# Kernel optimization log

Measured on AMD Instinct MI355X. Metric: run time of the kernel, lower is better.

Reference implementation:

```python
import jax, jax.numpy as jnp
import numpy as np

B, S, D, H = 4, 2048, 512, 8
KD = D // H          # key_dim == head_dim == 64
FFN = 4 * D

def _ln(x, g, b, eps):
    mu = x.mean(-1, keepdims=True)
    var = ((x - mu) ** 2).mean(-1, keepdims=True)
    return (x - mu) / jnp.sqrt(var + eps) * g + b

def setup_inputs():
    key = jax.random.key(0)
    ks = jax.random.split(key, 8)
    def lin(k, o, i, scale=0.02):
        k1, k2 = jax.random.split(k)
        return (jax.random.normal(k1, (o, i), jnp.float32) * scale,
                jax.random.normal(k2, (o,), jnp.float32) * scale)
    wq, bq = lin(ks[0], D, D)
    wk, bk = lin(ks[1], D, D)
    wv, bv = lin(ks[2], D, D)
    wg, bg = lin(ks[3], D, D)
    wo, bo = lin(ks[4], D, D)
    fc1_w, fc1_b = lin(ks[5], FFN, D)
    fc2_w, fc2_b = lin(ks[6], D, FFN)
    return {
        'src': jax.random.normal(ks[7], (B, S, D), jnp.float32),
        'mask': jnp.zeros((S, S), jnp.bool_),
        'padding_mask': jnp.zeros((B, S), jnp.bool_),
        'wq': wq, 'bq': bq, 'wk': wk, 'bk': bk, 'wv': wv, 'bv': bv,
        'wg': wg, 'bg': bg, 'wo': wo, 'bo': bo,
        'fc1_w': fc1_w, 'fc1_b': fc1_b, 'fc2_w': fc2_w, 'fc2_b': fc2_b,
        'ln_ffn_g': jnp.ones((FFN,), jnp.float32), 'ln_ffn_b': jnp.zeros((FFN,), jnp.float32),
        'n0_g': jnp.ones((D,), jnp.float32), 'n0_b': jnp.zeros((D,), jnp.float32),
        'n1_g': jnp.ones((D,), jnp.float32), 'n1_b': jnp.zeros((D,), jnp.float32),
    }

def reference(src, mask, padding_mask, wq, bq, wk, bk, wv, bv, wg, bg, wo, bo,
              fc1_w, fc1_b, fc2_w, fc2_b, ln_ffn_g, ln_ffn_b, n0_g, n0_b, n1_g, n1_b):
    b, s, d = src.shape
    # RetNet per-head decay mask (h, s, s): exp((i-j)*log(gamma_h)) on the lower triangle,
    # row-normalized by sqrt(row sum) (torchscale RetNetRelPos, parallel mode).
    idx = jnp.arange(s)
    diff = (idx[:, None] - idx[None, :]).astype(src.dtype)
    decay = jnp.log(1.0 - 2.0 ** (-5.0 - jnp.arange(H, dtype=src.dtype)))
    dm = jnp.where(diff[None] >= 0, jnp.exp(diff[None] * decay[:, None, None]), 0.0)
    dm = dm / jnp.sqrt(dm.sum(-1, keepdims=True))
    # projections; k scaled by key_dim**-0.5 before head split
    q = (src @ wq.T + bq).reshape(b, s, H, KD).transpose(0, 2, 1, 3)
    k = ((src @ wk.T + bk) * (KD ** -0.5)).reshape(b, s, H, KD).transpose(0, 2, 1, 3)
    v = src @ wv.T + bv
    g = src @ wg.T + bg
    # parallel retention: additive decay bias, detached L1 row normalization
    qk = jnp.einsum('bhid,bhjd->bhij', q, k) + dm[None]
    den = jnp.maximum(jnp.abs(jax.lax.stop_gradient(qk).sum(-1, keepdims=True)), 1.0)
    qk = qk / den
    vr = v.reshape(b, s, H, KD).transpose(0, 2, 1, 3)
    o = jnp.einsum('bhij,bhjd->bhid', qk, vr).transpose(0, 2, 1, 3)  # (b,s,h,hd)
    # per-head LayerNorm, eps=1e-6, no affine
    mu = o.mean(-1, keepdims=True)
    o = (o - mu) / jnp.sqrt(((o - mu) ** 2).mean(-1, keepdims=True) + 1e-6)
    o = jax.nn.silu(g) * o.reshape(b, s, d)
    o = o @ wo.T + bo
    # post-norm residual layout
    x = _ln(src + o, n0_g, n0_b, 1e-5)
    h = jax.nn.gelu(x @ fc1_w.T + fc1_b, approximate=False)
    h = _ln(h, ln_ffn_g, ln_ffn_b, 1e-6)  # subln
    h = h @ fc2_w.T + fc2_b
    return _ln(x + h, n1_g, n1_b, 1e-5)
```

## Files before the change

kernel.cpp:

```cpp
#include <hip/hip_runtime.h>
#include <hip/hip_bf16.h>
#include <math.h>

#define DEV __device__ __forceinline__

typedef __attribute__((ext_vector_type(4))) float f32x4;
typedef __attribute__((ext_vector_type(16))) float f32x16;
typedef __attribute__((ext_vector_type(8))) short bf16x8;
typedef __attribute__((ext_vector_type(8))) unsigned short u16x8;
typedef unsigned short u16;
typedef unsigned int u32;

DEV u16 f2bf(float f) {
  union { float f; u32 u; } v; v.f = f;
  u32 r = v.u + 0x7fffu + ((v.u >> 16) & 1u);
  return (u16)(r >> 16);
}
DEV float bf2f(u16 h) {
  union { u32 u; float f; } v; v.u = ((u32)h) << 16;
  return v.f;
}
DEV float bfel(bf16x8 v, int e) {
  union { bf16x8 b; u16x8 u; } x; x.b = v; return bf2f(x.u[e]);
}

DEV void gl_lds16(const u16* g, u16* s) {
  __builtin_amdgcn_global_load_lds((const __attribute__((address_space(1))) void*)g,
                                   (__attribute__((address_space(3))) void*)s, 16, 0, 0);
}

DEV void barrier_() {
  __builtin_amdgcn_sched_barrier(0);
  asm volatile("" ::: "memory");
  __builtin_amdgcn_s_barrier();
  asm volatile("" ::: "memory");
  __builtin_amdgcn_sched_barrier(0);
}

#define MFMA16(a, b, c) __builtin_amdgcn_mfma_f32_16x16x32_bf16((a), (b), (c), 0, 0, 0)
#define MFMA32(a, b, c) __builtin_amdgcn_mfma_f32_32x32x16_bf16((a), (b), (c), 0, 0, 0)

DEV void cast8(const float* in, u16* out, float s) {
  f32x4 a = *(const f32x4*)in;
  f32x4 b = *(const f32x4*)(in + 4);
  u16x8 r;
  r[0] = f2bf(a[0] * s); r[1] = f2bf(a[1] * s); r[2] = f2bf(a[2] * s); r[3] = f2bf(a[3] * s);
  r[4] = f2bf(b[0] * s); r[5] = f2bf(b[1] * s); r[6] = f2bf(b[2] * s); r[7] = f2bf(b[3] * s);
  *(u16x8*)out = r;
}

__global__ __launch_bounds__(256) void prep_cast(
    const float* __restrict__ src, const float* __restrict__ wq, const float* __restrict__ wk,
    const float* __restrict__ wv, const float* __restrict__ wg, const float* __restrict__ wo,
    const float* __restrict__ fc1, const float* __restrict__ fc2,
    const float* __restrict__ bq, const float* __restrict__ bk,
    const float* __restrict__ bv, const float* __restrict__ bg,
    u16* __restrict__ src_bf, u16* __restrict__ Wcat, u16* __restrict__ wo_bf,
    u16* __restrict__ fc1_bf, u16* __restrict__ fc2_bf, float* __restrict__ bcat) {
  int u = blockIdx.x * 256 + threadIdx.x;
  if (u < 524288) {
    cast8(src + (size_t)u * 8, src_bf + (size_t)u * 8, 1.0f);
  } else if (u < 557056) {
    int v = u - 524288; cast8(wq + (size_t)v * 8, Wcat + (size_t)v * 8, 1.0f);
  } else if (u < 589824) {
    int v = u - 557056; cast8(wk + (size_t)v * 8, Wcat + 262144 + (size_t)v * 8, 0.125f);
  } else if (u < 622592) {
    int v = u - 589824; cast8(wv + (size_t)v * 8, Wcat + 524288 + (size_t)v * 8, 1.0f);
  } else if (u < 655360) {
    int v = u - 622592; cast8(wg + (size_t)v * 8, Wcat + 786432 + (size_t)v * 8, 1.0f);
  } else if (u < 688128) {
    int v = u - 655360; cast8(wo + (size_t)v * 8, wo_bf + (size_t)v * 8, 1.0f);
  } else if (u < 819200) {
    int v = u - 688128; cast8(fc1 + (size_t)v * 8, fc1_bf + (size_t)v * 8, 1.0f);
  } else if (u < 950272) {
    int v = u - 819200; cast8(fc2 + (size_t)v * 8, fc2_bf + (size_t)v * 8, 1.0f);
  } else if (u < 950528) {
    int v = u - 950272;
    #pragma unroll
    for (int e = 0; e < 8; e++) {
      int c = v * 8 + e;
      float val;
      if (c < 512)       val = bq[c];
      else if (c < 1024) val = bk[c - 512] * 0.125f;
      else if (c < 1536) val = bv[c - 1024];
      else               val = bg[c - 1536];
      bcat[c] = val;
    }
  }
}

template <int ACT>
__global__ __launch_bounds__(256) void gemm_v4(
    const u16* __restrict__ A, const u16* __restrict__ W, const float* __restrict__ bias,
    u16* __restrict__ Ob, int N, int K, int TN) {
  __shared__ __align__(16) u16 sm[16384];
  const int t = threadIdx.x, l = t & 63;
  const int w = t >> 6, wr = (w >> 1) * 64, wc = (w & 1) * 64;
  const int lc = l & 15, lch = l >> 4;
  const int NT = K >> 5;

  const int orig = blockIdx.x;
  const int cpx = gridDim.x >> 3;
  const int sid = (orig & 7) * cpx + (orig >> 3);
  const int bm = (sid / TN) * 128, bn = (sid % TN) * 128;

  const int srow = t >> 2, sc = t & 3;
  const int soff = (sc ^ ((srow >> 1) & 3)) * 8;
  const u16* stA = A + (size_t)(bm + srow) * K + soff;
  const u16* stB = W + (size_t)(bn + srow) * K + soff;
  const size_t rstep = (size_t)64 * K;

#define STAGE(bidx, kt)                                   \
  {                                                       \
    u16* d = sm + (bidx) * 8192 + t * 8;                  \
    gl_lds16(stA + (kt), d);                              \
    gl_lds16(stA + rstep + (kt), d + 2048);               \
    gl_lds16(stB + (kt), d + 4096);                       \
    gl_lds16(stB + rstep + (kt), d + 6144);               \
  }

  f32x4 acc[4][4] = {};
  STAGE(0, 0)

  const int key = (lch ^ ((lc >> 1) & 3)) * 8;
  for (int tt = 0; tt < NT; ++tt) {
    if (tt + 1 < NT) {
      STAGE((tt + 1) & 1, (tt + 1) * 32)
      asm volatile("s_waitcnt vmcnt(4)" ::: "memory");
    } else {
      asm volatile("s_waitcnt vmcnt(0)" ::: "memory");
    }
    barrier_();
    const u16* bufp = sm + (tt & 1) * 8192;
    bf16x8 af[4], bfv[4];
    #pragma unroll
    for (int mi = 0; mi < 4; mi++)
      af[mi] = *(const bf16x8*)&bufp[(wr + mi * 16 + lc) * 32 + key];
    #pragma unroll
    for (int ni = 0; ni < 4; ni++)
      bfv[ni] = *(const bf16x8*)&bufp[4096 + (wc + ni * 16 + lc) * 32 + key];
    #pragma unroll
    for (int mi = 0; mi < 4; mi++)
      #pragma unroll
      for (int ni = 0; ni < 4; ni++)
        acc[mi][ni] = MFMA16(af[mi], bfv[ni], acc[mi][ni]);
    asm volatile("s_waitcnt lgkmcnt(0)" ::: "memory");
    barrier_();
  }
#undef STAGE

  u16* osm = sm;
  #pragma unroll
  for (int ni = 0; ni < 4; ni++) {
    const int col = wc + ni * 16 + lc;
    const float bb = bias[bn + col];
    const int ckey = col >> 3, clow = col & 7;
    #pragma unroll
    for (int mi = 0; mi < 4; mi++) {
      #pragma unroll
      for (int r = 0; r < 4; r++) {
        const int row = wr + mi * 16 + lch * 4 + r;
        float v = acc[mi][ni][r] + bb;
        if (ACT == 1) v = 0.5f * v * (1.0f + erff(v * 0.70710678118f));
        osm[row * 128 + ((ckey ^ ((row & 7) << 1)) << 3) + clow] = f2bf(v);
      }
    }
  }
  __syncthreads();
  #pragma unroll
  for (int p = 0; p < 8; p++) {
    const int flat = p * 256 + t;
    const int row = flat >> 4, c = flat & 15;
    u16x8 y = *(const u16x8*)&osm[row * 128 + ((c ^ ((row & 7) << 1)) << 3)];
    *(u16x8*)&Ob[(size_t)(bm + row) * N + bn + c * 8] = y;
  }
}

template <int ACT>
__global__ __launch_bounds__(256) void gemm_m64_v4(
    const u16* __restrict__ A, const u16* __restrict__ W, const float* __restrict__ bias,
    u16* __restrict__ Ob, int N, int K, int TN) {
  __shared__ __align__(16) u16 sm[12288];
  const int t = threadIdx.x, l = t & 63;
  const int w = t >> 6, wr = (w >> 1) * 32, wc = (w & 1) * 64;
  const int lc = l & 15, lch = l >> 4;
  const int NT = K >> 5;

  const int orig = blockIdx.x;
  const int cpx = gridDim.x >> 3;
  const int sid = (orig & 7) * cpx + (orig >> 3);
  const int bm = (sid / TN) * 64, bn = (sid % TN) * 128;

  const int srow = t >> 2, sc = t & 3;
  const int soff = (sc ^ ((srow >> 1) & 3)) * 8;
  const u16* stA = A + (size_t)(bm + srow) * K + soff;
  const u16* stB = W + (size_t)(bn + srow) * K + soff;
  const size_t rstep = (size_t)64 * K;

#define STAGE(bidx, kt)                                   \
  {                                                       \
    u16* d = sm + (bidx) * 6144 + t * 8;                  \
    gl_lds16(stA + (kt), d);                              \
    gl_lds16(stB + (kt), d + 2048);                       \
    gl_lds16(stB + rstep + (kt), d + 4096);               \
  }

  f32x4 acc[2][4] = {};
  STAGE(0, 0)

  const int key = (lch ^ ((lc >> 1) & 3)) * 8;
  for (int tt = 0; tt < NT; ++tt) {
    if (tt + 1 < NT) {
      STAGE((tt + 1) & 1, (tt + 1) * 32)
      asm volatile("s_waitcnt vmcnt(3)" ::: "memory");
    } else {
      asm volatile("s_waitcnt vmcnt(0)" ::: "memory");
    }
    barrier_();
    const u16* bufp = sm + (tt & 1) * 6144;
    bf16x8 af[2], bfv[4];
    #pragma unroll
    for (int mi = 0; mi < 2; mi++)
      af[mi] = *(const bf16x8*)&bufp[(wr + mi * 16 + lc) * 32 + key];
    #pragma unroll
    for (int ni = 0; ni < 4; ni++)
      bfv[ni] = *(const bf16x8*)&bufp[2048 + (wc + ni * 16 + lc) * 32 + key];
    #pragma unroll
    for (int mi = 0; mi < 2; mi++)
      #pragma unroll
      for (int ni = 0; ni < 4; ni++)
        acc[mi][ni] = MFMA16(af[mi], bfv[ni], acc[mi][ni]);
    asm volatile("s_waitcnt lgkmcnt(0)" ::: "memory");
    barrier_();
  }
#undef STAGE

  u16* osm = sm;
  #pragma unroll
  for (int ni = 0; ni < 4; ni++) {
    const int col = wc + ni * 16 + lc;
    const float bb = bias[bn + col];
    const int ckey = col >> 3, clow = col & 7;
    #pragma unroll
    for (int mi = 0; mi < 2; mi++) {
      #pragma unroll
      for (int r = 0; r < 4; r++) {
        const int row = wr + mi * 16 + lch * 4 + r;
        float v = acc[mi][ni][r] + bb;
        if (ACT == 1) v = 0.5f * v * (1.0f + erff(v * 0.70710678118f));
        osm[row * 128 + ((ckey ^ ((row & 7) << 1)) << 3) + clow] = f2bf(v);
      }
    }
  }
  __syncthreads();
  #pragma unroll
  for (int p = 0; p < 4; p++) {
    const int flat = p * 256 + t;
    const int row = flat >> 4, c = flat & 15;
    u16x8 y = *(const u16x8*)&osm[row * 128 + ((c ^ ((row & 7) << 1)) << 3)];
    *(u16x8*)&Ob[(size_t)(bm + row) * N + bn + c * 8] = y;
  }
}

__global__ __launch_bounds__(256) void transkv(
    const u16* __restrict__ qkvg, u16* __restrict__ ktg, u16* __restrict__ vtg,
    float* __restrict__ Wtab) {
  __shared__ u16 Lk[64 * 72], Lv[64 * 72];
  const int t = threadIdx.x;
  const int bh = blockIdx.x, c = blockIdx.y, b = bh >> 3, h = bh & 7;
  const int jt = c * 64;
  const u16* kptr = qkvg + (size_t)(b * 2048 + jt) * 2048 + 512 + h * 64;
  const u16* vptr = kptr + 512;
  const int r0 = t >> 3, c0 = (t & 7) * 8;
  u16x8 k0 = *(const u16x8*)(kptr + (size_t)r0 * 2048 + c0);
  u16x8 k1 = *(const u16x8*)(kptr + (size_t)(r0 + 32) * 2048 + c0);
  u16x8 v0 = *(const u16x8*)(vptr + (size_t)r0 * 2048 + c0);
  u16x8 v1 = *(const u16x8*)(vptr + (size_t)(r0 + 32) * 2048 + c0);
  #pragma unroll
  for (int e = 0; e < 8; e++) {
    Lk[(c0 + e) * 72 + r0] = k0[e];  Lk[(c0 + e) * 72 + 32 + r0] = k1[e];
    Lv[(c0 + e) * 72 + r0] = v0[e];  Lv[(c0 + e) * 72 + 32 + r0] = v1[e];
  }
  __syncthreads();
  {
    u16* kd = ktg + (size_t)bh * 64 * 2048 + jt;
    u16* vd = vtg + (size_t)bh * 64 * 2048 + jt;
    *(u16x8*)(kd + (size_t)r0 * 2048 + c0)        = *(const u16x8*)&Lk[r0 * 72 + c0];
    *(u16x8*)(kd + (size_t)(r0 + 32) * 2048 + c0) = *(const u16x8*)&Lk[(r0 + 32) * 72 + c0];
    *(u16x8*)(vd + (size_t)r0 * 2048 + c0)        = *(const u16x8*)&Lv[r0 * 72 + c0];
    *(u16x8*)(vd + (size_t)(r0 + 32) * 2048 + c0) = *(const u16x8*)&Lv[(r0 + 32) * 72 + c0];
  }
  if (t < 64) {
    const float gamma = 1.0f - exp2f(-5.0f - (float)h);
    float acc = 0.0f, p = 1.0f;
    for (int jj = 0; jj < 64; jj++) {
      acc += p * bf2f(Lv[t * 72 + (63 - jj)]);
      p *= gamma;
    }
    Wtab[((size_t)bh * 32 + c) * 64 + t] = acc;
  }
}

__global__ __launch_bounds__(256) void scan_kernel(
    const u16* __restrict__ ktg, float* __restrict__ Ctab, float* __restrict__ ksum) {
  __shared__ float ps[4][64];
  const int t = threadIdx.x, bh = blockIdx.x, h = bh & 7;
  const int a = t & 63, q = t >> 6;
  const u16* kr = ktg + (size_t)bh * 64 * 2048 + (size_t)a * 2048 + q * 512;
  float s = 0.0f;
  for (int j = 0; j < 512; j += 8) {
    u16x8 v = *(const u16x8*)(kr + j);
    #pragma unroll
    for (int e = 0; e < 8; e++) s += bf2f(v[e]);
  }
  ps[q][a] = s;
  __syncthreads();
  if (t < 64) {
    ksum[bh * 64 + t] = ps[0][t] + ps[1][t] + ps[2][t] + ps[3][t];
    const float gamma = 1.0f - exp2f(-5.0f - (float)h);
    const float g64 = exp2f(64.0f * log2f(gamma));
    float* Wp = Ctab + (size_t)bh * 32 * 64 + t;
    float C = 0.0f;
    for (int c = 0; c < 32; c++) {
      C = C * g64 + Wp[c * 64];
      Wp[c * 64] = C;
    }
  }
}

__global__ __launch_bounds__(256) void vtk_kernel(
    const u16* __restrict__ vtg, const u16* __restrict__ ktg, u16* __restrict__ vtk) {
  __shared__ float red[3][4096];
  const int t = threadIdx.x, l = t & 63, w = t >> 6;
  const int bh = blockIdx.x;
  const int lc = l & 15, lch = l >> 4;
  const u16* vb = vtg + (size_t)bh * 64 * 2048;
  const u16* kb = ktg + (size_t)bh * 64 * 2048;
  f32x4 acc[4][4] = {};
  for (int it = 0; it < 16; ++it) {
    const int j0 = w * 512 + it * 32 + lch * 8;
    bf16x8 af[4], bfr[4];
    #pragma unroll
    for (int mt = 0; mt < 4; mt++)
      af[mt] = *(const bf16x8*)(vb + (size_t)(mt * 16 + lc) * 2048 + j0);
    #pragma unroll
    for (int nt = 0; nt < 4; nt++)
      bfr[nt] = *(const bf16x8*)(kb + (size_t)(nt * 16 + lc) * 2048 + j0);
    #pragma unroll
    for (int mt = 0; mt < 4; mt++)
      #pragma unroll
      for (int nt = 0; nt < 4; nt++)
        acc[mt][nt] = MFMA16(af[mt], bfr[nt], acc[mt][nt]);
  }
  if (w > 0) {
    #pragma unroll
    for (int mt = 0; mt < 4; mt++)
      #pragma unroll
      for (int nt = 0; nt < 4; nt++)
        #pragma unroll
        for (int r = 0; r < 4; r++)
          red[w - 1][(mt * 16 + lch * 4 + r) * 64 + nt * 16 + lc] = acc[mt][nt][r];
  }
  __syncthreads();
  if (w == 0) {
    u16* out = vtk + (size_t)bh * 64 * 64;
    #pragma unroll
    for (int mt = 0; mt < 4; mt++)
      #pragma unroll
      for (int nt = 0; nt < 4; nt++)
        #pragma unroll
        for (int r = 0; r < 4; r++) {
          int row = mt * 16 + lch * 4 + r, col = nt * 16 + lc;
          float v = acc[mt][nt][r] + red[0][row * 64 + col] + red[1][row * 64 + col] +
                    red[2][row * 64 + col];
          out[row * 64 + col] = f2bf(v);
        }
  }
}

__global__ __launch_bounds__(512) void ret_out(
    const u16* __restrict__ qkvg, const u16* __restrict__ vtg,
    const u16* __restrict__ vtk, const float* __restrict__ Ctab,
    const float* __restrict__ ksum, u16* __restrict__ gated) {
  const int S = 2048, DD = 2048;
  const int bh = blockIdx.x, b = bh >> 3, h = bh & 7;
  const int t = threadIdx.x, l = t & 63, w = t >> 6;
  const int lid = l & 31, hi = l >> 5;
  const int wrow = blockIdx.y * 256 + w * 32;
  const int i_q = wrow + lid;
  const int chunk = wrow >> 6;
  const int iloc = i_q & 63;

  __shared__ __align__(16) u16 sm[18432];
  float* smf = (float*)sm;

  const size_t base = (size_t)b * S * DD + (size_t)h * 64;
  const u16* qp = qkvg + base;
  const u16* gp = qkvg + base + 1536;

  const float gamma = 1.0f - exp2f(-5.0f - (float)h);
  const float l2g = log2f(gamma);
  const float rowsum = (1.0f - exp2f((float)(i_q + 1) * l2g)) * exp2f(5.0f + (float)h);
  const float rrs = rsqrtf(rowsum);

  {
    const int il = t >> 3, j0 = (t & 7) * 8;
    u16x8 row;
    #pragma unroll
    for (int e = 0; e < 8; e++) {
      int d = il - (j0 + e);
      row[e] = (d >= 0) ? f2bf(exp2f((float)d * l2g)) : (u16)0;
    }
    *(u16x8*)&sm[il * 72 + j0] = row;
  }
  if (t < 256) {
    int cc = blockIdx.y * 4 - 1 + (t >> 6);
    smf[4608 + t] = (cc >= 0) ? Ctab[((size_t)bh * 32 + cc) * 64 + (t & 63)] : 0.0f;
  } else if (t < 320) {
    smf[4864 + (t - 256)] = ksum[bh * 64 + (t - 256)];
  }
  __syncthreads();

  bf16x8 qf[4];
  #pragma unroll
  for (int kc = 0; kc < 4; kc++)
    qf[kc] = *(const bf16x8*)(qp + (size_t)i_q * DD + kc * 16 + 8 * hi);

  const u16* vt_b = vtg + (size_t)bh * 64 * S;
  const u16* vk_b = vtk + (size_t)bh * 64 * 64;

  f32x16 accO0, accO1;
  #pragma unroll
  for (int r = 0; r < 16; r++) { accO0[r] = 0.0f; accO1[r] = 0.0f; }

  #pragma unroll
  for (int kc = 0; kc < 4; kc++) {
    bf16x8 lb = *(const bf16x8*)&sm[iloc * 72 + kc * 16 + hi * 8];
    bf16x8 va0 = *(const bf16x8*)(vt_b + (size_t)lid * S + chunk * 64 + kc * 16 + hi * 8);
    bf16x8 va1 = *(const bf16x8*)(vt_b + (size_t)(lid + 32) * S + chunk * 64 + kc * 16 + hi * 8);
    accO0 = MFMA32(va0, lb, accO0);
    accO1 = MFMA32(va1, lb, accO1);
  }
  {
    const float gpw = exp2f((float)(iloc + 1) * l2g);
    const float* Cst = &smf[4608 + (w >> 1) * 64];
    #pragma unroll
    for (int r = 0; r < 16; r++) {
      int br = (r & 3) + 8 * (r >> 2) + 4 * hi;
      accO0[r] += gpw * Cst[br];
      accO1[r] += gpw * Cst[32 + br];
    }
  }
  #pragma unroll
  for (int r = 0; r < 16; r++) { accO0[r] *= rrs; accO1[r] *= rrs; }
  #pragma unroll
  for (int kc = 0; kc < 4; kc++) {
    bf16x8 ka0 = *(const bf16x8*)(vk_b + (size_t)lid * 64 + kc * 16 + hi * 8);
    bf16x8 ka1 = *(const bf16x8*)(vk_b + (size_t)(lid + 32) * 64 + kc * 16 + hi * 8);
    accO0 = MFMA32(ka0, qf[kc], accO0);
    accO1 = MFMA32(ka1, qf[kc], accO1);
  }
  float dsum = 0.0f;
  #pragma unroll
  for (int kc = 0; kc < 4; kc++) {
    const float* Ks = &smf[4864 + kc * 16 + hi * 8];
    #pragma unroll
    for (int e = 0; e < 8; e++) dsum += bfel(qf[kc], e) * Ks[e];
  }
  dsum += __shfl_xor(dsum, 32);
  float den = dsum + sqrtf(rowsum);
  float rden = 1.0f / fmaxf(fabsf(den), 1.0f);

  float o0[16], o1[16];
  float s1 = 0.0f, s2 = 0.0f;
  #pragma unroll
  for (int r = 0; r < 16; r++) {
    o0[r] = accO0[r] * rden; s1 += o0[r]; s2 += o0[r] * o0[r];
    o1[r] = accO1[r] * rden; s1 += o1[r]; s2 += o1[r] * o1[r];
  }
  s1 += __shfl_xor(s1, 32);
  s2 += __shfl_xor(s2, 32);
  float mu = s1 * (1.0f / 64.0f);
  float var = s2 * (1.0f / 64.0f) - mu * mu;
  float rv = rsqrtf(var + 1e-6f);

  __syncthreads();

  u16* Ot = sm + w * 2304;
  #pragma unroll
  for (int r = 0; r < 16; r++) {
    int d = (r & 3) + 8 * (r >> 2) + 4 * hi;
    Ot[lid * 72 + d]      = f2bf((o0[r] - mu) * rv);
    Ot[lid * 72 + 32 + d] = f2bf((o1[r] - mu) * rv);
  }
  {
    const int i2 = l >> 1, half = l & 1;
    const int row = wrow + i2;
    #pragma unroll
    for (int c = 0; c < 4; c++) {
      u16x8 y8 = *(const u16x8*)&Ot[i2 * 72 + half * 32 + c * 8];
      u16x8 g8 = *(const u16x8*)(gp + (size_t)row * DD + half * 32 + c * 8);
      u16x8 o8;
      #pragma unroll
      for (int e = 0; e < 8; e++) {
        float gv = bf2f(g8[e]);
        float sg = gv / (1.0f + __expf(-gv));
        o8[e] = f2bf(bf2f(y8[e]) * sg);
      }
      *(u16x8*)&gated[((size_t)(b * S + row)) * 512 + h * 64 + half * 32 + c * 8] = o8;
    }
  }
}

template <int AF32, int WF>
__global__ __launch_bounds__(256) void add_lnT(
    const void* __restrict__ Ap, const u16* __restrict__ Bv,
    const float* __restrict__ gam, const float* __restrict__ bet, float eps,
    float* __restrict__ Of, u16* __restrict__ Ob) {
  int row = blockIdx.x * 4 + (threadIdx.x >> 6);
  int l = threadIdx.x & 63;
  float x[8];
  u16x8 cv = *(const u16x8*)(Bv + (size_t)row * 512 + l * 8);
  if (AF32) {
    const float* a = (const float*)Ap + (size_t)row * 512 + l * 8;
    f32x4 a0 = *(const f32x4*)a, a1 = *(const f32x4*)(a + 4);
    #pragma unroll
    for (int e = 0; e < 4; e++) { x[e] = a0[e] + bf2f(cv[e]); x[4 + e] = a1[e] + bf2f(cv[4 + e]); }
  } else {
    u16x8 av = *(const u16x8*)((const u16*)Ap + (size_t)row * 512 + l * 8);
    #pragma unroll
    for (int e = 0; e < 8; e++) x[e] = bf2f(av[e]) + bf2f(cv[e]);
  }
  float s = 0.f, s2 = 0.f;
  #pragma unroll
  for (int e = 0; e < 8; e++) { s += x[e]; s2 += x[e] * x[e]; }
  #pragma unroll
  for (int m = 1; m <= 32; m <<= 1) { s += __shfl_xor(s, m); s2 += __shfl_xor(s2, m); }
  float mu = s * (1.0f / 512.0f);
  float var = s2 * (1.0f / 512.0f) - mu * mu;
  float rinv = rsqrtf(var + eps);
  f32x4 g0 = *(const f32x4*)(gam + l * 8), g1 = *(const f32x4*)(gam + l * 8 + 4);
  f32x4 b0 = *(const f32x4*)(bet + l * 8), b1 = *(const f32x4*)(bet + l * 8 + 4);
  f32x4 y0, y1;
  #pragma unroll
  for (int e = 0; e < 4; e++) {
    y0[e] = (x[e] - mu) * rinv * g0[e] + b0[e];
    y1[e] = (x[4 + e] - mu) * rinv * g1[e] + b1[e];
  }
  if (WF) {
    float* op = Of + (size_t)row * 512 + l * 8;
    *(f32x4*)op = y0;
    *(f32x4*)(op + 4) = y1;
  }
  if (Ob) {
    u16x8 rb_;
    #pragma unroll
    for (int e = 0; e < 4; e++) { rb_[e] = f2bf(y0[e]); rb_[4 + e] = f2bf(y1[e]); }
    *(u16x8*)(Ob + (size_t)row * 512 + l * 8) = rb_;
  }
}

__global__ __launch_bounds__(256) void subln_ffn(
    u16* __restrict__ hbuf, const float* __restrict__ gam, const float* __restrict__ bet) {
  int row = blockIdx.x * 4 + (threadIdx.x >> 6);
  int l = threadIdx.x & 63;
  u16* p = hbuf + (size_t)row * 2048;
  float x[32];
  #pragma unroll
  for (int cch = 0; cch < 4; cch++) {
    u16x8 v = *(const u16x8*)(p + cch * 512 + l * 8);
    #pragma unroll
    for (int e = 0; e < 8; e++) x[cch * 8 + e] = bf2f(v[e]);
  }
  float s = 0.f, s2 = 0.f;
  #pragma unroll
  for (int e = 0; e < 32; e++) { s += x[e]; s2 += x[e] * x[e]; }
  #pragma unroll
  for (int m = 1; m <= 32; m <<= 1) { s += __shfl_xor(s, m); s2 += __shfl_xor(s2, m); }
  float mu = s * (1.0f / 2048.0f);
  float var = s2 * (1.0f / 2048.0f) - mu * mu;
  float rinv = rsqrtf(var + 1e-6f);
  #pragma unroll
  for (int cch = 0; cch < 4; cch++) {
    int col = cch * 512 + l * 8;
    f32x4 g0 = *(const f32x4*)(gam + col), g1 = *(const f32x4*)(gam + col + 4);
    f32x4 b0 = *(const f32x4*)(bet + col), b1 = *(const f32x4*)(bet + col + 4);
    u16x8 o;
    #pragma unroll
    for (int e = 0; e < 4; e++) {
      o[e]     = f2bf((x[cch * 8 + e]     - mu) * rinv * g0[e] + b0[e]);
      o[4 + e] = f2bf((x[cch * 8 + 4 + e] - mu) * rinv * g1[e] + b1[e]);
    }
    *(u16x8*)(p + col) = o;
  }
}

extern "C" void kernel_launch(void* const* d_in, const int* in_sizes, int n_in,
                              void* d_out, int out_size, void* d_ws, size_t ws_size,
                              hipStream_t stream) {
  const float* src  = (const float*)d_in[0];
  const float* wq   = (const float*)d_in[3];
  const float* bq   = (const float*)d_in[4];
  const float* wk   = (const float*)d_in[5];
  const float* bk   = (const float*)d_in[6];
  const float* wv   = (const float*)d_in[7];
  const float* bv   = (const float*)d_in[8];
  const float* wg   = (const float*)d_in[9];
  const float* bg   = (const float*)d_in[10];
  const float* wo   = (const float*)d_in[11];
  const float* bo   = (const float*)d_in[12];
  const float* fc1w = (const float*)d_in[13];
  const float* fc1b = (const float*)d_in[14];
  const float* fc2w = (const float*)d_in[15];
  const float* fc2b = (const float*)d_in[16];
  const float* lng  = (const float*)d_in[17];
  const float* lnb  = (const float*)d_in[18];
  const float* n0g  = (const float*)d_in[19];
  const float* n0b  = (const float*)d_in[20];
  const float* n1g  = (const float*)d_in[21];
  const float* n1b  = (const float*)d_in[22];

  if (ws_size < 91242496u) return;

  char* ws = (char*)d_ws;
  u16*   src_bf = (u16*)(ws + 0);
  u16*   Wcat   = (u16*)(ws + 8388608);
  u16*   wo_bf  = (u16*)(ws + 10485760);
  u16*   fc1_bf = (u16*)(ws + 11010048);
  u16*   fc2_bf = (u16*)(ws + 13107200);
  float* bcat   = (float*)(ws + 15204352);
  u16*   qkvg   = (u16*)(ws + 15212544);
  u16*   gated  = (u16*)(ws + 48766976);
  u16*   attn   = (u16*)(ws + 57155584);
  u16*   vtg    = (u16*)(ws + 65544192);
  u16*   ktg    = (u16*)(ws + 73932800);
  u16*   xbf    = (u16*)(ws + 82321408);
  float* Ctab   = (float*)(ws + 90710016);
  u16*   vtkb   = (u16*)(ws + 90972160);
  float* ksumb  = (float*)(ws + 91234304);

  prep_cast<<<3713, 256, 0, stream>>>(src, wq, wk, wv, wg, wo, fc1w, fc2w,
                                      bq, bk, bv, bg,
                                      src_bf, Wcat, wo_bf, fc1_bf, fc2_bf, bcat);
  gemm_v4<0><<<1024, 256, 0, stream>>>(src_bf, Wcat, bcat, qkvg, 2048, 512, 16);
  transkv<<<dim3(32, 32), 256, 0, stream>>>(qkvg, ktg, vtg, Ctab);
  scan_kernel<<<32, 256, 0, stream>>>(ktg, Ctab, ksumb);
  vtk_kernel<<<32, 256, 0, stream>>>(vtg, ktg, vtkb);
  ret_out<<<dim3(32, 8), 512, 0, stream>>>(qkvg, vtg, vtkb, Ctab, ksumb, gated);
  gemm_m64_v4<0><<<512, 256, 0, stream>>>(gated, wo_bf, bo, attn, 512, 512, 4);
  add_lnT<1, 0><<<2048, 256, 0, stream>>>(src, attn, n0g, n0b, 1e-5f, nullptr, xbf);
  gemm_v4<1><<<1024, 256, 0, stream>>>(xbf, fc1_bf, fc1b, qkvg, 2048, 512, 16);
  subln_ffn<<<2048, 256, 0, stream>>>(qkvg, lng, lnb);
  gemm_m64_v4<0><<<512, 256, 0, stream>>>(qkvg, fc2_bf, fc2b, attn, 512, 2048, 4);
  add_lnT<0, 1><<<2048, 256, 0, stream>>>(xbf, attn, n1g, n1b, 1e-5f, (float*)d_out, nullptr);
}
```

Before: 187.8 us.

## Replace double-buffered GEMMs with direct-A-load GEMM holding full W slice in LDS

Result: slower. 246.9 us (+31.5%).

```diff
diff --git a/kernel.cpp b/kernel.cpp
--- a/kernel.cpp
+++ b/kernel.cpp
@@ -27,14 +27,6 @@
 DEV void gl_lds16(const u16* g, u16* s) {
   __builtin_amdgcn_global_load_lds((const __attribute__((address_space(1))) void*)g,
                                    (__attribute__((address_space(3))) void*)s, 16, 0, 0);
-}
-
-DEV void barrier_() {
-  __builtin_amdgcn_sched_barrier(0);
-  asm volatile("" ::: "memory");
-  __builtin_amdgcn_s_barrier();
-  asm volatile("" ::: "memory");
-  __builtin_amdgcn_sched_barrier(0);
 }
 
 #define MFMA16(a, b, c) __builtin_amdgcn_mfma_f32_16x16x32_bf16((a), (b), (c), 0, 0, 0)
@@ -89,80 +81,72 @@
   }
 }
 
-template <int ACT>
-__global__ __launch_bounds__(256) void gemm_v4(
+template <int ACT, int NSEC>
+__global__ __launch_bounds__(256) void gemm_direct(
     const u16* __restrict__ A, const u16* __restrict__ W, const float* __restrict__ bias,
     u16* __restrict__ Ob, int N, int K, int TN) {
-  __shared__ __align__(16) u16 sm[16384];
-  const int t = threadIdx.x, l = t & 63;
-  const int w = t >> 6, wr = (w >> 1) * 64, wc = (w & 1) * 64;
+  __shared__ __align__(16) u16 sm[32768];
+  const int t = threadIdx.x, l = t & 63, w = t >> 6;
   const int lc = l & 15, lch = l >> 4;
-  const int NT = K >> 5;
 
   const int orig = blockIdx.x;
   const int cpx = gridDim.x >> 3;
   const int sid = (orig & 7) * cpx + (orig >> 3);
-  const int bm = (sid / TN) * 128, bn = (sid % TN) * 128;
-
-  const int srow = t >> 2, sc = t & 3;
-  const int soff = (sc ^ ((srow >> 1) & 3)) * 8;
-  const u16* stA = A + (size_t)(bm + srow) * K + soff;
-  const u16* stB = W + (size_t)(bn + srow) * K + soff;
-  const size_t rstep = (size_t)64 * K;
-
-#define STAGE(bidx, kt)                                   \
-  {                                                       \
-    u16* d = sm + (bidx) * 8192 + t * 8;                  \
-    gl_lds16(stA + (kt), d);                              \
-    gl_lds16(stA + rstep + (kt), d + 2048);               \
-    gl_lds16(stB + (kt), d + 4096);                       \
-    gl_lds16(stB + rstep + (kt), d + 6144);               \
-  }
+  const int bm = (sid / TN) * 256, bn = (sid % TN) * 64;
 
   f32x4 acc[4][4] = {};
-  STAGE(0, 0)
-
-  const int key = (lch ^ ((lc >> 1) & 3)) * 8;
-  for (int tt = 0; tt < NT; ++tt) {
-    if (tt + 1 < NT) {
-      STAGE((tt + 1) & 1, (tt + 1) * 32)
-      asm volatile("s_waitcnt vmcnt(4)" ::: "memory");
-    } else {
-      asm volatile("s_waitcnt vmcnt(0)" ::: "memory");
-    }
-    barrier_();
-    const u16* bufp = sm + (tt & 1) * 8192;
-    bf16x8 af[4], bfv[4];
-    #pragma unroll
-    for (int mi = 0; mi < 4; mi++)
-      af[mi] = *(const bf16x8*)&bufp[(wr + mi * 16 + lc) * 32 + key];
-    #pragma unroll
-    for (int ni = 0; ni < 4; ni++)
-      bfv[ni] = *(const bf16x8*)&bufp[4096 + (wc + ni * 16 + lc) * 32 + key];
-    #pragma unroll
-    for (int mi = 0; mi < 4; mi++)
-      #pragma unroll
-      for (int ni = 0; ni < 4; ni++)
-        acc[mi][ni] = MFMA16(af[mi], bfv[ni], acc[mi][ni]);
-    asm volatile("s_waitcnt lgkmcnt(0)" ::: "memory");
-    barrier_();
-  }
-#undef STAGE
-
+
+  const u16* Abase = A + (size_t)(bm + w * 64 + lc) * K;
+
+  for (int sec = 0; sec < NSEC; ++sec) {
+    if (sec > 0) __syncthreads();
+    #pragma unroll
+    for (int p = 0; p < 16; ++p) {
+      const int flat = p * 256 + t;
+      const int row = flat >> 6, ch = flat & 63;
+      gl_lds16(W + (size_t)(bn + row) * K + sec * 512 + ((ch ^ (row & 7)) * 8),
+               sm + flat * 8);
+    }
+    asm volatile("s_waitcnt vmcnt(0)" ::: "memory");
+    __syncthreads();
+
+    const u16* Ap = Abase + sec * 512;
+    #pragma unroll 4
+    for (int tt = 0; tt < 16; ++tt) {
+      const int kb = tt * 32 + lch * 8;
+      bf16x8 af[4], bfv[4];
+      #pragma unroll
+      for (int mi = 0; mi < 4; mi++)
+        af[mi] = *(const bf16x8*)(Ap + (size_t)(mi * 16) * K + kb);
+      #pragma unroll
+      for (int ni = 0; ni < 4; ni++) {
+        const int r = ni * 16 + lc;
+        const int c = tt * 4 + lch;
+        bfv[ni] = *(const bf16x8*)&sm[r * 512 + ((c ^ (r & 7)) * 8)];
+      }
+      #pragma unroll
+      for (int mi = 0; mi < 4; mi++)
+        #pragma unroll
+        for (int ni = 0; ni < 4; ni++)
+          acc[mi][ni] = MFMA16(af[mi], bfv[ni], acc[mi][ni]);
+    }
+  }
+
+  __syncthreads();
   u16* osm = sm;
   #pragma unroll
   for (int ni = 0; ni < 4; ni++) {
-    const int col = wc + ni * 16 + lc;
+    const int col = ni * 16 + lc;
     const float bb = bias[bn + col];
-    const int ckey = col >> 3, clow = col & 7;
+    const int cch = col >> 3, clow = col & 7;
     #pragma unroll
     for (int mi = 0; mi < 4; mi++) {
       #pragma unroll
       for (int r = 0; r < 4; r++) {
-        const int row = wr + mi * 16 + lch * 4 + r;
+        const int row = w * 64 + mi * 16 + lch * 4 + r;
         float v = acc[mi][ni][r] + bb;
         if (ACT == 1) v = 0.5f * v * (1.0f + erff(v * 0.70710678118f));
-        osm[row * 128 + ((ckey ^ ((row & 7) << 1)) << 3) + clow] = f2bf(v);
+        osm[row * 64 + ((cch ^ (row & 7)) << 3) + clow] = f2bf(v);
       }
     }
   }
@@ -170,94 +154,8 @@
   #pragma unroll
   for (int p = 0; p < 8; p++) {
     const int flat = p * 256 + t;
-    const int row = flat >> 4, c = flat & 15;
-    u16x8 y = *(const u16x8*)&osm[row * 128 + ((c ^ ((row & 7) << 1)) << 3)];
-    *(u16x8*)&Ob[(size_t)(bm + row) * N + bn + c * 8] = y;
-  }
-}
-
-template <int ACT>
-__global__ __launch_bounds__(256) void gemm_m64_v4(
-    const u16* __restrict__ A, const u16* __restrict__ W, const float* __restrict__ bias,
-    u16* __restrict__ Ob, int N, int K, int TN) {
-  __shared__ __align__(16) u16 sm[12288];
-  const int t = threadIdx.x, l = t & 63;
-  const int w = t >> 6, wr = (w >> 1) * 32, wc = (w & 1) * 64;
-  const int lc = l & 15, lch = l >> 4;
-  const int NT = K >> 5;
-
-  const int orig = blockIdx.x;
-  const int cpx = gridDim.x >> 3;
-  const int sid = (orig & 7) * cpx + (orig >> 3);
-  const int bm = (sid / TN) * 64, bn = (sid % TN) * 128;
-
-  const int srow = t >> 2, sc = t & 3;
-  const int soff = (sc ^ ((srow >> 1) & 3)) * 8;
-  const u16* stA = A + (size_t)(bm + srow) * K + soff;
-  const u16* stB = W + (size_t)(bn + srow) * K + soff;
-  const size_t rstep = (size_t)64 * K;
-
-#define STAGE(bidx, kt)                                   \
-  {                                                       \
-    u16* d = sm + (bidx) * 6144 + t * 8;                  \
-    gl_lds16(stA + (kt), d);                              \
-    gl_lds16(stB + (kt), d + 2048);                       \
-    gl_lds16(stB + rstep + (kt), d + 4096);               \
-  }
-
-  f32x4 acc[2][4] = {};
-  STAGE(0, 0)
-
-  const int key = (lch ^ ((lc >> 1) & 3)) * 8;
-  for (int tt = 0; tt < NT; ++tt) {
-    if (tt + 1 < NT) {
-      STAGE((tt + 1) & 1, (tt + 1) * 32)
-      asm volatile("s_waitcnt vmcnt(3)" ::: "memory");
-    } else {
-      asm volatile("s_waitcnt vmcnt(0)" ::: "memory");
-    }
-    barrier_();
-    const u16* bufp = sm + (tt & 1) * 6144;
-    bf16x8 af[2], bfv[4];
-    #pragma unroll
-    for (int mi = 0; mi < 2; mi++)
-      af[mi] = *(const bf16x8*)&bufp[(wr + mi * 16 + lc) * 32 + key];
-    #pragma unroll
-    for (int ni = 0; ni < 4; ni++)
-      bfv[ni] = *(const bf16x8*)&bufp[2048 + (wc + ni * 16 + lc) * 32 + key];
-    #pragma unroll
-    for (int mi = 0; mi < 2; mi++)
-      #pragma unroll
-      for (int ni = 0; ni < 4; ni++)
-        acc[mi][ni] = MFMA16(af[mi], bfv[ni], acc[mi][ni]);
-    asm volatile("s_waitcnt lgkmcnt(0)" ::: "memory");
-    barrier_();
-  }
-#undef STAGE
-
-  u16* osm = sm;
-  #pragma unroll
-  for (int ni = 0; ni < 4; ni++) {
-    const int col = wc + ni * 16 + lc;
-    const float bb = bias[bn + col];
-    const int ckey = col >> 3, clow = col & 7;
-    #pragma unroll
-    for (int mi = 0; mi < 2; mi++) {
-      #pragma unroll
-      for (int r = 0; r < 4; r++) {
-        const int row = wr + mi * 16 + lch * 4 + r;
-        float v = acc[mi][ni][r] + bb;
-        if (ACT == 1) v = 0.5f * v * (1.0f + erff(v * 0.70710678118f));
-        osm[row * 128 + ((ckey ^ ((row & 7) << 1)) << 3) + clow] = f2bf(v);
-      }
-    }
-  }
-  __syncthreads();
-  #pragma unroll
-  for (int p = 0; p < 4; p++) {
-    const int flat = p * 256 + t;
-    const int row = flat >> 4, c = flat & 15;
-    u16x8 y = *(const u16x8*)&osm[row * 128 + ((c ^ ((row & 7) << 1)) << 3)];
+    const int row = flat >> 3, c = flat & 7;
+    u16x8 y = *(const u16x8*)&osm[row * 64 + ((c ^ (row & 7)) << 3)];
     *(u16x8*)&Ob[(size_t)(bm + row) * N + bn + c * 8] = y;
   }
 }
@@ -642,15 +540,15 @@
   prep_cast<<<3713, 256, 0, stream>>>(src, wq, wk, wv, wg, wo, fc1w, fc2w,
                                       bq, bk, bv, bg,
                                       src_bf, Wcat, wo_bf, fc1_bf, fc2_bf, bcat);
-  gemm_v4<0><<<1024, 256, 0, stream>>>(src_bf, Wcat, bcat, qkvg, 2048, 512, 16);
+  gemm_direct<0, 1><<<1024, 256, 0, stream>>>(src_bf, Wcat, bcat, qkvg, 2048, 512, 32);
   transkv<<<dim3(32, 32), 256, 0, stream>>>(qkvg, ktg, vtg, Ctab);
   scan_kernel<<<32, 256, 0, stream>>>(ktg, Ctab, ksumb);
   vtk_kernel<<<32, 256, 0, stream>>>(vtg, ktg, vtkb);
   ret_out<<<dim3(32, 8), 512, 0, stream>>>(qkvg, vtg, vtkb, Ctab, ksumb, gated);
-  gemm_m64_v4<0><<<512, 256, 0, stream>>>(gated, wo_bf, bo, attn, 512, 512, 4);
+  gemm_direct<0, 1><<<256, 256, 0, stream>>>(gated, wo_bf, bo, attn, 512, 512, 8);
   add_lnT<1, 0><<<2048, 256, 0, stream>>>(src, attn, n0g, n0b, 1e-5f, nullptr, xbf);
-  gemm_v4<1><<<1024, 256, 0, stream>>>(xbf, fc1_bf, fc1b, qkvg, 2048, 512, 16);
+  gemm_direct<1, 1><<<1024, 256, 0, stream>>>(xbf, fc1_bf, fc1b, qkvg, 2048, 512, 32);
   subln_ffn<<<2048, 256, 0, stream>>>(qkvg, lng, lnb);
-  gemm_m64_v4<0><<<512, 256, 0, stream>>>(qkvg, fc2_bf, fc2b, attn, 512, 2048, 4);
+  gemm_direct<0, 4><<<256, 256, 0, stream>>>(qkvg, fc2_bf, fc2b, attn, 512, 2048, 8);
   add_lnT<0, 1><<<2048, 256, 0, stream>>>(xbf, attn, n1g, n1b, 1e-5f, (float*)d_out, nullptr);
 }
```
